# Kernel optimization log

Measured on AMD Instinct MI355X. Metric: run time of the kernel, lower is better.

## Reference

```python
import jax, jax.numpy as jnp
import numpy as np

NPOINT = 1024   # samples (farthest point sampling count)
RADIUS = 0.2    # ball query radius
K = 32          # neighbors per ball


def farthest_point_sample(xyz, npoint):
    # xyz: [B, N, 3] -> idx: [B, npoint] int32
    B, N, _ = xyz.shape
    def body(carry, _):
        dists, farthest = carry                      # [B,N], [B]
        centroid = jnp.take_along_axis(xyz, farthest[:, None, None], axis=1)  # [B,1,3]
        d = jnp.sum((xyz - centroid) ** 2, axis=-1)  # [B,N]
        dists = jnp.minimum(dists, d)
        nxt = jnp.argmax(dists, axis=-1).astype(jnp.int32)
        return (dists, nxt), farthest
    init = (jnp.full((B, N), 1e10, dtype=xyz.dtype), jnp.zeros((B,), jnp.int32))
    _, idx = jax.lax.scan(body, init, None, length=npoint)
    return jnp.transpose(idx)  # [B, npoint]


def query_ball_point(radius, k, xyz, new_xyz):
    # returns idx: [B, S, k] int32 -- first k in-radius point indices,
    # padded with the first found index (TF query_ball_point semantics)
    N = xyz.shape[1]
    sqd = jnp.sum((new_xyz[:, :, None, :] - xyz[:, None, :, :]) ** 2, axis=-1)  # [B,S,N]
    cand = jnp.where(sqd <= radius * radius, jnp.arange(N, dtype=jnp.int32)[None, None, :], N)
    idx = jnp.sort(cand, axis=-1)[..., :k]          # [B,S,k]
    first = idx[..., :1]
    return jnp.where(idx == N, first, idx).astype(jnp.int32)


def group_point(x, idx):
    # x: [B,N,C], idx: [B,S,k] -> [B,S,k,C]
    return jax.vmap(lambda xb, ib: xb[ib])(x, idx)


def setup_inputs() -> dict:
    key = jax.random.key(0)
    ks = jax.random.split(key, 8)
    B, N, C = 16, 4096, 64
    xyz = jax.random.uniform(ks[0], (B, N, 3), dtype=jnp.float32)
    points = jax.random.normal(ks[1], (B, N, C), dtype=jnp.float32)
    cin = 3 + C  # use_xyz concat
    widths = [64, 64, 128]
    W, b, c = [], [], cin
    for i, w in enumerate(widths):
        W.append(jax.random.normal(ks[2 + i], (c, w), dtype=jnp.float32) * (1.0 / np.sqrt(c)))
        b.append(jnp.zeros((w,), dtype=jnp.float32))
        c = w
    return {"xyz": xyz, "points": points,
            "W0": W[0], "b0": b[0], "W1": W[1], "b1": b[1], "W2": W[2], "b2": b[2]}


def reference(xyz, points, W0, b0, W1, b1, W2, b2):
    # --- sample_and_group ---
    fps_idx = farthest_point_sample(xyz, NPOINT)                 # [B,S]
    new_xyz = jax.vmap(lambda xb, ib: xb[ib])(xyz, fps_idx)      # [B,S,3]
    idx = query_ball_point(RADIUS, K, xyz, new_xyz)              # [B,S,K]
    grouped_xyz = group_point(xyz, idx) - new_xyz[:, :, None, :] # [B,S,K,3]
    grouped_points = group_point(points, idx)                    # [B,S,K,C]
    new_points = jnp.concatenate([grouped_xyz, grouped_points], axis=-1)  # [B,S,K,3+C]
    # --- shared 1x1-conv MLP (bn=False, relu) ---
    for W, bb in ((W0, b0), (W1, b1), (W2, b2)):
        new_points = jax.nn.relu(jnp.einsum('bskc,cd->bskd', new_points, W) + bb)
    # --- max pool over neighborhood ---
    new_points = jnp.max(new_points, axis=2)                     # [B,S,Cout]
    return new_xyz, new_points, idx
```

## Files before the change

kernel.cpp:

```cpp
#include <hip/hip_runtime.h>

#define BB 16
#define NN 4096
#define SS 1024
#define KNB 32
#define FPT 16
#define FNW 4

typedef unsigned long long ull;
typedef float v2f __attribute__((ext_vector_type(2)));

__device__ __forceinline__ float sqd3(float dx, float dy, float dz) {
    return __fadd_rn(__fadd_rn(__fmul_rn(dx, dx), __fmul_rn(dy, dy)), __fmul_rn(dz, dz));
}

#define DPPMAX(m, ctrl, rm)                                                              \
    {                                                                                    \
        unsigned _t = (unsigned)__builtin_amdgcn_update_dpp((int)(m), (int)(m), (ctrl),  \
                                                            (rm), 0xf, false);           \
        (m) = ((m) > _t) ? (m) : _t;                                                     \
    }

__global__ __launch_bounds__(256) void fused1_kernel(const float* __restrict__ xyz,
                                                     const float* __restrict__ points,
                                                     const float* __restrict__ W0,
                                                     const float* __restrict__ b0,
                                                     float* __restrict__ P1,
                                                     float4* __restrict__ xyz4,
                                                     float* __restrict__ out_newxyz) {
    __shared__ union {
        struct {
            float4 pts4[NN];
            ull    keys[2][FNW];
            int    hist[SS];
        } f;
        float w0s[67 * 64];
    } sm;

    const int t = threadIdx.x;

    if (blockIdx.x < BB) {
        const int b = blockIdx.x;
        const int lane = t & 63;
        const float* src = xyz + (size_t)b * (NN * 3) + (size_t)t * (FPT * 3);

        v2f px2[8], py2[8], pz2[8], d2[8];
        {
            float c48[48];
#pragma unroll
            for (int m = 0; m < 12; ++m) {
                float4 v = ((const float4*)src)[m];
                c48[4 * m + 0] = v.x; c48[4 * m + 1] = v.y;
                c48[4 * m + 2] = v.z; c48[4 * m + 3] = v.w;
            }
#pragma unroll
            for (int j = 0; j < 8; ++j) {
                px2[j] = (v2f){c48[6 * j + 0], c48[6 * j + 3]};
                py2[j] = (v2f){c48[6 * j + 1], c48[6 * j + 4]};
                pz2[j] = (v2f){c48[6 * j + 2], c48[6 * j + 5]};
                d2[j]  = (v2f){1e10f, 1e10f};
                sm.f.pts4[t * FPT + 2 * j + 0] = make_float4(px2[j].x, py2[j].x, pz2[j].x, 0.f);
                sm.f.pts4[t * FPT + 2 * j + 1] = make_float4(px2[j].y, py2[j].y, pz2[j].y, 0.f);
            }
        }
        __syncthreads();

        int far = 0;
        for (int it = 0; it < SS; ++it) {
            if (t == 0) sm.f.hist[it] = far;
            if (it == SS - 1) break;
            float4 c = sm.f.pts4[far];

            float bv0 = -1.f, bv1 = -1.f;
            int bn0 = 0, bn1 = 0;
            {
#pragma clang fp contract(off)
                v2f cx2 = {c.x, c.x}, cy2 = {c.y, c.y}, cz2 = {c.z, c.z};
#pragma unroll
                for (int j = 0; j < 4; ++j) {
                    v2f dx = px2[j] - cx2;
                    v2f dy = py2[j] - cy2;
                    v2f dz = pz2[j] - cz2;
                    v2f s = (dx * dx + dy * dy) + dz * dz;
                    float d0 = fminf(d2[j].x, s.x);
                    float d1 = fminf(d2[j].y, s.y);
                    d2[j] = (v2f){d0, d1};
                    bool g0 = d0 > bv0; bv0 = g0 ? d0 : bv0; bn0 = g0 ? (t * FPT + 2 * j + 0) : bn0;
                    bool g1 = d1 > bv0; bv0 = g1 ? d1 : bv0; bn0 = g1 ? (t * FPT + 2 * j + 1) : bn0;
                }
#pragma unroll
                for (int j = 4; j < 8; ++j) {
                    v2f dx = px2[j] - cx2;
                    v2f dy = py2[j] - cy2;
                    v2f dz = pz2[j] - cz2;
                    v2f s = (dx * dx + dy * dy) + dz * dz;
                    float d0 = fminf(d2[j].x, s.x);
                    float d1 = fminf(d2[j].y, s.y);
                    d2[j] = (v2f){d0, d1};
                    bool g0 = d0 > bv1; bv1 = g0 ? d0 : bv1; bn1 = g0 ? (t * FPT + 2 * j + 0) : bn1;
                    bool g1 = d1 > bv1; bv1 = g1 ? d1 : bv1; bn1 = g1 ? (t * FPT + 2 * j + 1) : bn1;
                }
            }
            bool gm = bv1 > bv0;
            float bv = gm ? bv1 : bv0;
            int bn = gm ? bn1 : bn0;

            unsigned mb = __float_as_uint(bv);
            DPPMAX(mb, 0x111, 0xf);
            DPPMAX(mb, 0x112, 0xf);
            DPPMAX(mb, 0x114, 0xf);
            DPPMAX(mb, 0x118, 0xf);
            DPPMAX(mb, 0x142, 0xa);
            DPPMAX(mb, 0x143, 0xc);
            unsigned vmb = (unsigned)__builtin_amdgcn_readlane((int)mb, 63);

            ull ball = __ballot(__float_as_uint(bv) == vmb);
            int sel = __ffsll(ball) - 1;
            int widx = __builtin_amdgcn_readlane(bn, sel);

            const int par = it & 1;
            if (lane == 0) {
                sm.f.keys[par][t >> 6] = ((ull)vmb << 32) | (unsigned)(~widx);
            }
            __syncthreads();
            ulonglong2 ka = *(const ulonglong2*)&sm.f.keys[par][0];
            ulonglong2 kb = *(const ulonglong2*)&sm.f.keys[par][2];
            ull a0 = (ka.x > ka.y) ? ka.x : ka.y;
            ull a1 = (kb.x > kb.y) ? kb.x : kb.y;
            ull best = (a0 > a1) ? a0 : a1;
            far = (int)(~(unsigned)best);
        }
        __syncthreads();
#pragma unroll
        for (int r = 0; r < 4; ++r) {
            int it2 = t + 256 * r;
            int fi = sm.f.hist[it2];
            float4 c = sm.f.pts4[fi];
            size_t o = ((size_t)b * SS + it2) * 3;
            out_newxyz[o + 0] = c.x;
            out_newxyz[o + 1] = c.y;
            out_newxyz[o + 2] = c.z;
        }
    } else {
        for (int i = t; i < 67 * 64; i += 256) sm.w0s[i] = W0[i];
        __syncthreads();
        const int lane = t & 63;
        const int wv = t >> 6;

        {
            int n0 = (blockIdx.x - BB) * 256 + t;
            xyz4[n0] = make_float4(xyz[3 * n0 + 0], xyz[3 * n0 + 1], xyz[3 * n0 + 2], 0.f);
        }

        const float bias = b0[lane];
        const int base = (blockIdx.x - BB) * 256 + wv * 64;
        for (int pi = 0; pi < 64; ++pi) {
            const int n = base + pi;
            const float* xp = xyz + (size_t)n * 3;
            const float* pp = points + (size_t)n * 64;
            float acc = bias;
            acc = fmaf(xp[0], sm.w0s[0 * 64 + lane], acc);
            acc = fmaf(xp[1], sm.w0s[1 * 64 + lane], acc);
            acc = fmaf(xp[2], sm.w0s[2 * 64 + lane], acc);
#pragma unroll 8
            for (int c = 0; c < 64; ++c) acc = fmaf(pp[c], sm.w0s[(3 + c) * 64 + lane], acc);
            P1[(size_t)n * 64 + lane] = acc;
        }
    }
}

__global__ __launch_bounds__(256) void k3_kernel(const float4* __restrict__ xyz4,
                                                 const float* __restrict__ P1,
                                                 const float* __restrict__ W0,
                                                 const float* __restrict__ W1,
                                                 const float* __restrict__ b1,
                                                 const float* __restrict__ W2,
                                                 const float* __restrict__ b2,
                                                 float* __restrict__ d_out) {
    const int t = threadIdx.x;
    const int lane = t & 63;
    const int wv = t >> 6;
    const int b = blockIdx.x >> 10;

    __shared__ int   ids[KNB];
    __shared__ int   bq[2][FNW];
    __shared__ float part[4][128];
    __shared__ float hs[4][8][64];

    float* out_newxyz = d_out;
    float* out_points = d_out + (size_t)BB * SS * 3;
    float* out_idx    = d_out + (size_t)BB * SS * 3 + (size_t)BB * SS * 128;

    const size_t q = (size_t)blockIdx.x;
    const float nx = out_newxyz[q * 3 + 0];
    const float ny = out_newxyz[q * 3 + 1];
    const float nz = out_newxyz[q * 3 + 2];

    const float qv = nx * W0[lane] + ny * W0[64 + lane] + nz * W0[128 + lane];
    float w1col[64];
#pragma unroll
    for (int i = 0; i < 64; ++i) w1col[i] = W1[i * 64 + lane];
    const float b1v = b1[lane];

    {
        const float4* xb4 = xyz4 + (size_t)b * NN;
        const float R2 = 0.04f;
        const ull ltm = (1ull << lane) - 1ull;
        int total = 0, c0 = 0, pr = 0;
        float4 pc = xb4[t];
        while (true) {
            float4 cur = pc;
            int nc0 = c0 + 256;
            if (nc0 < NN) pc = xb4[nc0 + t];
            float d = sqd3(cur.x - nx, cur.y - ny, cur.z - nz);
            bool in = (d <= R2);
            ull m = __ballot(in);
            if (lane == 0) bq[pr][wv] = __popcll(m);
            __syncthreads();
            int q0 = bq[pr][0], q1 = bq[pr][1], q2 = bq[pr][2], q3 = bq[pr][3];
            int basew = total + (wv > 0 ? q0 : 0) + (wv > 1 ? q1 : 0) + (wv > 2 ? q2 : 0);
            int pos = basew + __popcll(m & ltm);
            if (in && pos < KNB) ids[pos] = c0 + t;
            total += q0 + q1 + q2 + q3;
            c0 = nc0;
            pr ^= 1;
            if (total >= KNB || c0 >= NN) break;
        }
        __syncthreads();
        int cnt = (total < KNB) ? total : KNB;
        if (t >= cnt && t < KNB) ids[t] = ids[0];
    }
    __syncthreads();
    if (t < KNB) out_idx[q * KNB + t] = (float)ids[t];

    const float* P1b = P1 + (size_t)b * NN * 64;
#pragma unroll
    for (int kk = 0; kk < 8; ++kk) {
        int n = ids[wv * 8 + kk];
        float v = P1b[(size_t)n * 64 + lane] - qv;
        hs[wv][kk][lane] = fmaxf(v, 0.f);
    }

    float acc[8];
#pragma unroll
    for (int kk = 0; kk < 8; ++kk) acc[kk] = b1v;
#pragma unroll
    for (int qd = 0; qd < 16; ++qd) {
#pragma unroll
        for (int kk = 0; kk < 8; ++kk) {
            float4 h4 = *(const float4*)&hs[wv][kk][4 * qd];
            acc[kk] = fmaf(h4.x, w1col[4 * qd + 0], acc[kk]);
            acc[kk] = fmaf(h4.y, w1col[4 * qd + 1], acc[kk]);
            acc[kk] = fmaf(h4.z, w1col[4 * qd + 2], acc[kk]);
            acc[kk] = fmaf(h4.w, w1col[4 * qd + 3], acc[kk]);
        }
    }
#pragma unroll
    for (int kk = 0; kk < 8; ++kk) hs[wv][kk][lane] = fmaxf(acc[kk], 0.f);

    float outmax[2];
#pragma unroll
    for (int p = 0; p < 2; ++p) {
        float w2col[64];
#pragma unroll
        for (int i = 0; i < 64; ++i) w2col[i] = W2[i * 128 + 64 * p + lane];
        const float b2v = b2[64 * p + lane];
        float acc3[8];
#pragma unroll
        for (int kk = 0; kk < 8; ++kk) acc3[kk] = b2v;
#pragma unroll
        for (int qd = 0; qd < 16; ++qd) {
#pragma unroll
            for (int kk = 0; kk < 8; ++kk) {
                float4 h4 = *(const float4*)&hs[wv][kk][4 * qd];
                acc3[kk] = fmaf(h4.x, w2col[4 * qd + 0], acc3[kk]);
                acc3[kk] = fmaf(h4.y, w2col[4 * qd + 1], acc3[kk]);
                acc3[kk] = fmaf(h4.z, w2col[4 * qd + 2], acc3[kk]);
                acc3[kk] = fmaf(h4.w, w2col[4 * qd + 3], acc3[kk]);
            }
        }
        float m = 0.f;
#pragma unroll
        for (int kk = 0; kk < 8; ++kk) m = fmaxf(m, acc3[kk]);
        outmax[p] = m;
    }
    part[wv][lane] = outmax[0];
    part[wv][64 + lane] = outmax[1];
    __syncthreads();
    if (t < 128) {
        float v = fmaxf(fmaxf(part[0][t], part[1][t]), fmaxf(part[2][t], part[3][t]));
        out_points[q * 128 + t] = v;
    }
}

extern "C" void kernel_launch(void* const* d_in, const int* in_sizes, int n_in,
                              void* d_out, int out_size, void* d_ws, size_t ws_size,
                              hipStream_t stream) {
    const float* xyz    = (const float*)d_in[0];
    const float* points = (const float*)d_in[1];
    const float* W0     = (const float*)d_in[2];
    const float* b0     = (const float*)d_in[3];
    const float* W1     = (const float*)d_in[4];
    const float* b1     = (const float*)d_in[5];
    const float* W2     = (const float*)d_in[6];
    const float* b2     = (const float*)d_in[7];
    float* out = (float*)d_out;
    float*  P1   = (float*)d_ws;
    float4* xyz4 = (float4*)((char*)d_ws + (size_t)BB * NN * 64 * 4);

    hipLaunchKernelGGL(fused1_kernel, dim3(BB + (BB * NN) / 256), dim3(256), 0, stream,
                       xyz, points, W0, b0, P1, xyz4, out);
    hipLaunchKernelGGL(k3_kernel, dim3(BB * SS), dim3(256), 0, stream,
                       xyz4, P1, W0, W1, b1, W2, b2, out);
}
```

Before: 749.6 us.

## Use packed v2f FMAs and LDS-staged transposed W2 in k3 MLP

Rewrites the per-query MLP layers 2 and 3 in k3 to operate on pairs of neighbors with packed float2 FMA (v_pk_fma_f32), interleaving hidden activations as [lane][2] in LDS. W2 is transposed into padded shared memory at block start instead of being loaded per lane into 64 registers twice from global memory. The aim is to halve FMA instruction count and cut register pressure and redundant global weight loads. The cost is extra LDS traffic (about 35KB more shared memory per block, which may lower occupancy) and a per-block W2 staging loop.

```diff
diff --git a/kernel.cpp b/kernel.cpp
--- a/kernel.cpp
+++ b/kernel.cpp
@@ -182,10 +182,11 @@
     const int wv = t >> 6;
     const int b = blockIdx.x >> 10;
 
+    __shared__ float w2t[128][68];
+    __shared__ float hs2[4][4][64][2];
+    __shared__ float part[4][128];
     __shared__ int   ids[KNB];
     __shared__ int   bq[2][FNW];
-    __shared__ float part[4][128];
-    __shared__ float hs[4][8][64];
 
     float* out_newxyz = d_out;
     float* out_points = d_out + (size_t)BB * SS * 3;
@@ -195,6 +196,19 @@
     const float nx = out_newxyz[q * 3 + 0];
     const float ny = out_newxyz[q * 3 + 1];
     const float nz = out_newxyz[q * 3 + 2];
+
+#pragma unroll
+    for (int r = 0; r < 8; ++r) {
+        int m = t + 256 * r;
+        int o = m & 127;
+        int i4 = m >> 7;
+        float4 v;
+        v.x = W2[(4 * i4 + 0) * 128 + o];
+        v.y = W2[(4 * i4 + 1) * 128 + o];
+        v.z = W2[(4 * i4 + 2) * 128 + o];
+        v.w = W2[(4 * i4 + 3) * 128 + o];
+        *(float4*)&w2t[o][4 * i4] = v;
+    }
 
     const float qv = nx * W0[lane] + ny * W0[64 + lane] + nz * W0[128 + lane];
     float w1col[64];
@@ -235,57 +249,81 @@
 
     const float* P1b = P1 + (size_t)b * NN * 64;
 #pragma unroll
-    for (int kk = 0; kk < 8; ++kk) {
-        int n = ids[wv * 8 + kk];
-        float v = P1b[(size_t)n * 64 + lane] - qv;
-        hs[wv][kk][lane] = fmaxf(v, 0.f);
-    }
-
-    float acc[8];
-#pragma unroll
-    for (int kk = 0; kk < 8; ++kk) acc[kk] = b1v;
-#pragma unroll
-    for (int qd = 0; qd < 16; ++qd) {
-#pragma unroll
-        for (int kk = 0; kk < 8; ++kk) {
-            float4 h4 = *(const float4*)&hs[wv][kk][4 * qd];
-            acc[kk] = fmaf(h4.x, w1col[4 * qd + 0], acc[kk]);
-            acc[kk] = fmaf(h4.y, w1col[4 * qd + 1], acc[kk]);
-            acc[kk] = fmaf(h4.z, w1col[4 * qd + 2], acc[kk]);
-            acc[kk] = fmaf(h4.w, w1col[4 * qd + 3], acc[kk]);
-        }
-    }
-#pragma unroll
-    for (int kk = 0; kk < 8; ++kk) hs[wv][kk][lane] = fmaxf(acc[kk], 0.f);
-
-    float outmax[2];
-#pragma unroll
-    for (int p = 0; p < 2; ++p) {
-        float w2col[64];
-#pragma unroll
-        for (int i = 0; i < 64; ++i) w2col[i] = W2[i * 128 + 64 * p + lane];
-        const float b2v = b2[64 * p + lane];
-        float acc3[8];
-#pragma unroll
-        for (int kk = 0; kk < 8; ++kk) acc3[kk] = b2v;
+    for (int p = 0; p < 4; ++p) {
+        int n0 = ids[wv * 8 + 2 * p + 0];
+        int n1 = ids[wv * 8 + 2 * p + 1];
+        float v0_ = fmaxf(P1b[(size_t)n0 * 64 + lane] - qv, 0.f);
+        float v1_ = fmaxf(P1b[(size_t)n1 * 64 + lane] - qv, 0.f);
+        *(v2f*)&hs2[wv][p][lane][0] = (v2f){v0_, v1_};
+    }
+
+    {
+#pragma clang fp contract(fast)
+        v2f accp[4];
+#pragma unroll
+        for (int p = 0; p < 4; ++p) accp[p] = (v2f){b1v, b1v};
 #pragma unroll
         for (int qd = 0; qd < 16; ++qd) {
 #pragma unroll
-            for (int kk = 0; kk < 8; ++kk) {
-                float4 h4 = *(const float4*)&hs[wv][kk][4 * qd];
-                acc3[kk] = fmaf(h4.x, w2col[4 * qd + 0], acc3[kk]);
-                acc3[kk] = fmaf(h4.y, w2col[4 * qd + 1], acc3[kk]);
-                acc3[kk] = fmaf(h4.z, w2col[4 * qd + 2], acc3[kk]);
-                acc3[kk] = fmaf(h4.w, w2col[4 * qd + 3], acc3[kk]);
-            }
-        }
-        float m = 0.f;
-#pragma unroll
-        for (int kk = 0; kk < 8; ++kk) m = fmaxf(m, acc3[kk]);
-        outmax[p] = m;
-    }
-    part[wv][lane] = outmax[0];
-    part[wv][64 + lane] = outmax[1];
+            for (int i2 = 0; i2 < 2; ++i2) {
+                const int i = 4 * qd + 2 * i2;
+                v2f wlo = {w1col[i], w1col[i]};
+                v2f whi = {w1col[i + 1], w1col[i + 1]};
+#pragma unroll
+                for (int p = 0; p < 4; ++p) {
+                    float4 h4 = *(const float4*)&hs2[wv][p][i][0];
+                    v2f hA = {h4.x, h4.y};
+                    v2f hB = {h4.z, h4.w};
+                    accp[p] = hA * wlo + accp[p];
+                    accp[p] = hB * whi + accp[p];
+                }
+            }
+        }
+#pragma unroll
+        for (int p = 0; p < 4; ++p) {
+            v2f h2p;
+            h2p.x = fmaxf(accp[p].x, 0.f);
+            h2p.y = fmaxf(accp[p].y, 0.f);
+            *(v2f*)&hs2[wv][p][lane][0] = h2p;
+        }
+    }
+
+    float ma = 0.f, mbv = 0.f;
+    {
+#pragma clang fp contract(fast)
+        const float b2a = b2[lane];
+        const float b2bv = b2[64 + lane];
+        v2f a3[4], b3[4];
+#pragma unroll
+        for (int p = 0; p < 4; ++p) { a3[p] = (v2f){b2a, b2a}; b3[p] = (v2f){b2bv, b2bv}; }
+#pragma unroll
+        for (int qd = 0; qd < 16; ++qd) {
+            float4 wa4 = *(const float4*)&w2t[lane][4 * qd];
+            float4 wb4 = *(const float4*)&w2t[64 + lane][4 * qd];
+            v2f wax = {wa4.x, wa4.x}, way = {wa4.y, wa4.y};
+            v2f waz = {wa4.z, wa4.z}, waw = {wa4.w, wa4.w};
+            v2f wbx = {wb4.x, wb4.x}, wby = {wb4.y, wb4.y};
+            v2f wbz = {wb4.z, wb4.z}, wbw = {wb4.w, wb4.w};
+#pragma unroll
+            for (int p = 0; p < 4; ++p) {
+                float4 h0 = *(const float4*)&hs2[wv][p][4 * qd][0];
+                float4 h1_ = *(const float4*)&hs2[wv][p][4 * qd + 2][0];
+                v2f hA0 = {h0.x, h0.y},  hA1 = {h0.z, h0.w};
+                v2f hA2 = {h1_.x, h1_.y}, hA3 = {h1_.z, h1_.w};
+                a3[p] = hA0 * wax + a3[p];  b3[p] = hA0 * wbx + b3[p];
+                a3[p] = hA1 * way + a3[p];  b3[p] = hA1 * wby + b3[p];
+                a3[p] = hA2 * waz + a3[p];  b3[p] = hA2 * wbz + b3[p];
+                a3[p] = hA3 * waw + a3[p];  b3[p] = hA3 * wbw + b3[p];
+            }
+        }
+#pragma unroll
+        for (int p = 0; p < 4; ++p) {
+            ma = fmaxf(ma, fmaxf(a3[p].x, a3[p].y));
+            mbv = fmaxf(mbv, fmaxf(b3[p].x, b3[p].y));
+        }
+    }
+    part[wv][lane] = ma;
+    part[wv][64 + lane] = mbv;
     __syncthreads();
     if (t < 128) {
         float v = fmaxf(fmaxf(part[0][t], part[1][t]), fmaxf(part[2][t], part[3][t]));
```

Result: slower. 814.7 us (+8.7%).
